# Performance work log

Hardware: AMD Instinct MI355X
Metric: run time of the kernel (lower is better)

Reference implementation:

```python
import jax, jax.numpy as jnp
import numpy as np

N_HEADS = 32
N_KV_HEADS = 8
HEAD_DIM = 64
ROPE_BASE = 10000.0


def setup_inputs() -> dict:
    key = jax.random.key(0)
    ks = jax.random.split(key, 5)
    B, T, C = 4, 1024, 2048
    kv_dim = N_KV_HEADS * HEAD_DIM
    scale = 0.02
    return {
        "x": jax.random.normal(ks[0], (B, T, C), dtype=jnp.float32),
        "Wq": jax.random.normal(ks[1], (C, C), dtype=jnp.float32) * scale,
        "Wk": jax.random.normal(ks[2], (C, kv_dim), dtype=jnp.float32) * scale,
        "Wv": jax.random.normal(ks[3], (C, kv_dim), dtype=jnp.float32) * scale,
        "Wp": jax.random.normal(ks[4], (C, C), dtype=jnp.float32) * scale,
    }


def _rotate_half(x):
    # interleaved rotation: (x0,x1,x2,x3,...) -> (-x1,x0,-x3,x2,...)
    x1 = x[..., ::2]
    x2 = x[..., 1::2]
    return jnp.stack((-x2, x1), axis=-1).reshape(x.shape)


def _rope_tables(T, dtype):
    inv_freq = 1.0 / (ROPE_BASE ** (jnp.arange(0, HEAD_DIM, 2, dtype=jnp.float32) / HEAD_DIM))
    freqs = jnp.arange(T, dtype=jnp.float32)[:, None] * inv_freq[None, :]  # (T, D/2)
    cos = jnp.repeat(jnp.cos(freqs), 2, axis=-1).astype(dtype)  # (T, D)
    sin = jnp.repeat(jnp.sin(freqs), 2, axis=-1).astype(dtype)
    return cos[None, None], sin[None, None]  # (1,1,T,D)


def reference(x, Wq, Wk, Wv, Wp):
    B, T, C = x.shape
    H, KV, D = N_HEADS, N_KV_HEADS, HEAD_DIM
    q = (x @ Wq).reshape(B, T, H, D).transpose(0, 2, 1, 3)   # (B,H,T,D)
    k = (x @ Wk).reshape(B, T, KV, D).transpose(0, 2, 1, 3)  # (B,KV,T,D)
    v = (x @ Wv).reshape(B, T, KV, D).transpose(0, 2, 1, 3)

    cos, sin = _rope_tables(T, x.dtype)
    q = q * cos + _rotate_half(q) * sin
    k = k * cos + _rotate_half(k) * sin

    rf = H // KV
    k = jnp.repeat(k, rf, axis=1)  # (B,H,T,D) GQA broadcast
    v = jnp.repeat(v, rf, axis=1)

    scores = jnp.einsum('bhqd,bhkd->bhqk', q, k) / jnp.sqrt(jnp.asarray(D, x.dtype))
    causal = jnp.tril(jnp.ones((T, T), dtype=bool))
    scores = jnp.where(causal[None, None], scores, -jnp.inf)
    attn = jax.nn.softmax(scores, axis=-1)
    out = jnp.einsum('bhqk,bhkd->bhqd', attn, v)  # (B,H,T,D)
    out = out.transpose(0, 2, 1, 3).reshape(B, T, C)
    return out @ Wp
```

## Files before the change

### kernel.cpp

```cpp
#include <hip/hip_runtime.h>
#include <hip/hip_bf16.h>


typedef __attribute__((ext_vector_type(4))) float f32x4;
typedef __attribute__((ext_vector_type(8))) short short8;

#define AS1C(p) ((const __attribute__((address_space(1))) void*)(p))
#define AS3(p)  ((__attribute__((address_space(3))) void*)(p))

__device__ __forceinline__ unsigned short f2bf(float f) {
  union { float f; unsigned int u; } x; x.f = f;
  unsigned int r = x.u + 0x7FFFu + ((x.u >> 16) & 1u);
  return (unsigned short)(r >> 16);
}

__device__ __forceinline__ unsigned short bfc(float f) {
  return __bfloat16_as_ushort(__float2bfloat16(f));
}

__device__ __forceinline__ float ex2(float x) {
  return __builtin_amdgcn_exp2f(x);
}

__global__ void rope_tab_kernel(float2* __restrict__ tab) {
  const int idx = blockIdx.x * 256 + threadIdx.x;
  const int t = idx >> 5, i = idx & 31;
  const float invf = exp2f(-(float)i * 0.41524101186092029f);
  float sv, cv;
  __sincosf((float)t * invf, &sv, &cv);
  tab[idx] = make_float2(cv, sv);
}

__global__ void cvt_bf16_kernel(const float* __restrict__ src,
                                unsigned short* __restrict__ dst, int n4) {
  int i = blockIdx.x * blockDim.x + threadIdx.x;
  if (i >= n4) return;
  const f32x4 v = *(const f32x4*)(src + (size_t)i * 4);
  ushort4 u = make_ushort4(f2bf(v[0]), f2bf(v[1]), f2bf(v[2]), f2bf(v[3]));
  *(ushort4*)(dst + (size_t)i * 4) = u;
}

__global__ void transpose_qkv_w_kernel(const float* __restrict__ Wq,
                                       const float* __restrict__ Wk,
                                       const float* __restrict__ Wv,
                                       unsigned short* __restrict__ dst) {
  __shared__ float tile[32][33];
  const int z = blockIdx.z;
  const float* src;
  int N, rowOff;
  float scale;
  if (z == 0)      { src = Wq; N = 2048; rowOff = 0;    scale = 0.18033688011112042f; }
  else if (z == 1) { src = Wk; N = 512;  rowOff = 2048; scale = 1.0f; }
  else             { src = Wv; N = 512;  rowOff = 2560; scale = 1.0f; }
  const int n0 = blockIdx.x * 32, k0 = blockIdx.y * 32;
  if (n0 >= N) return;
  const int tx = threadIdx.x & 31, ty = threadIdx.x >> 5;
#pragma unroll
  for (int i = ty; i < 32; i += 8)
    tile[i][tx] = src[(size_t)(k0 + i) * N + (n0 + tx)];
  __syncthreads();
#pragma unroll
  for (int i = ty; i < 32; i += 8)
    dst[(size_t)(rowOff + n0 + i) * 2048 + (k0 + tx)] = f2bf(tile[tx][i] * scale);
}

__global__ void transpose_bf16_kernel(const float* __restrict__ src,
                                      unsigned short* __restrict__ dst,
                                      int N, int rowOff, float scale) {
  __shared__ float tile[32][33];
  const int n0 = blockIdx.x * 32, k0 = blockIdx.y * 32;
  const int tx = threadIdx.x & 31, ty = threadIdx.x >> 5;
#pragma unroll
  for (int i = ty; i < 32; i += 8)
    tile[i][tx] = src[(size_t)(k0 + i) * N + (n0 + tx)];
  __syncthreads();
#pragma unroll
  for (int i = ty; i < 32; i += 8)
    dst[(size_t)(rowOff + n0 + i) * 2048 + (k0 + tx)] = f2bf(tile[tx][i] * scale);
}

__global__ void rope_cvt2_kernel(const float2* __restrict__ tab,
                                 const float* __restrict__ qkf,
                                 unsigned short* __restrict__ qb,
                                 unsigned short* __restrict__ kb) {
  const int idx = blockIdx.x * 256 + threadIdx.x;
  const int m = idx / 320;
  const int p = idx - m * 320;
  const int t = m & 1023;
  unsigned short* dst;
  int srcCol, dcol;
  if (p < 256) { dcol = p * 8; srcCol = dcol; dst = qb + (size_t)m * 2048 + dcol; }
  else         { dcol = (p - 256) * 8; srcCol = 2048 + dcol; dst = kb + (size_t)m * 512 + dcol; }
  const int i0 = (srcCol & 63) >> 1;
  const float* src = qkf + (size_t)m * 2560 + srcCol;
  const f32x4 v0 = *(const f32x4*)(src);
  const f32x4 v1 = *(const f32x4*)(src + 4);
  float x[8] = {v0[0], v0[1], v0[2], v0[3], v1[0], v1[1], v1[2], v1[3]};
  short8 o;
#pragma unroll
  for (int j = 0; j < 4; ++j) {
    const float2 cs = tab[t * 32 + i0 + j];
    const float x1 = x[2 * j], x2 = x[2 * j + 1];
    o[2 * j]     = (short)bfc(x1 * cs.x - x2 * cs.y);
    o[2 * j + 1] = (short)bfc(x2 * cs.x + x1 * cs.y);
  }
  *(short8*)dst = o;
}

#define GEMM_CORE(A_, Bt_, K_)                                                           \
  __shared__ unsigned short S[65536];                                                    \
  const int tid = threadIdx.x;                                                           \
  const int lane = tid & 63, w = tid >> 6;                                               \
  const int l15 = lane & 15, lg = lane >> 4;                                             \
  const int nwgx = gridDim.x;                                                            \
  const int nwg = nwgx * gridDim.y;                                                      \
  int lid = blockIdx.x + nwgx * blockIdx.y;                                              \
  lid = (lid & 7) * (nwg >> 3) + (lid >> 3);                                             \
  const int m0 = (lid / nwgx) * 256, n0 = (lid % nwgx) * 256;                            \
  const int ah = w >> 2;                                                                 \
  const int bh = (w & 3) >> 1;                                                           \
  const int bs = (w & 1) * 64;                                                           \
  const int NT = (K_) >> 6;                                                              \
  const int sr = tid >> 3;                                                               \
  const int sc = ((tid & 7) ^ (sr & 7)) << 3;                                            \
  f32x4 acc[8][4];                                                                       \
  _Pragma("unroll") for (int i = 0; i < 8; ++i)                                          \
  _Pragma("unroll") for (int j = 0; j < 4; ++j)                                          \
  _Pragma("unroll") for (int c = 0; c < 4; ++c) acc[i][j][c] = 0.f;                      \
  SB(0, 0); SB(0, 1); SA(0, 0); SA(0, 1);                                                \
  SB(1, 0); SB(1, 1); SA(1, 0); SA(1, 1);                                                \
  asm volatile("s_waitcnt vmcnt(8)" ::: "memory");                                       \
  __builtin_amdgcn_s_barrier();                                                          \
  short8 af[2][4], b0[2][2], b1[2][2];                                                   \
  for (int t = 0; t < NT; t += 2) {                                                      \
    const bool nl = (t + 2 < NT);                                                        \
    RDA(t, 0); RDB(b0, t, 0);                                                            \
    BAR();                                                                               \
    MM(0, 0, b0);                                                                        \
    BAR();                                                                               \
    RDB(b1, t, 1);                                                                       \
    BAR();                                                                               \
    MM(0, 1, b1);                                                                        \
    BAR();                                                                               \
    RDA(t, 1);                                                                           \
    if (nl) SB(t + 2, 0);                                                                \
    BAR();                                                                               \
    MM(1, 1, b1);                                                                        \
    BAR();                                                                               \
    if (nl) {                                                                            \
      SB(t + 2, 1); SA(t + 2, 0);                                                        \
      asm volatile("s_waitcnt vmcnt(6)" ::: "memory");                                   \
    } else {                                                                             \
      asm volatile("s_waitcnt vmcnt(0)" ::: "memory");                                   \
    }                                                                                    \
    BAR();                                                                               \
    MM(1, 0, b0);                                                                        \
    BAR();                                                                               \
    RDA(t + 1, 0); RDB(b0, t + 1, 0);                                                    \
    if (nl) SA(t + 2, 1);                                                                \
    BAR();                                                                               \
    MM(0, 0, b0);                                                                        \
    BAR();                                                                               \
    RDB(b1, t + 1, 1);                                                                   \
    BAR();                                                                               \
    MM(0, 1, b1);                                                                        \
    BAR();                                                                               \
    RDA(t + 1, 1);                                                                       \
    if (nl) SB(t + 3, 0);                                                                \
    BAR();                                                                               \
    MM(1, 1, b1);                                                                        \
    BAR();                                                                               \
    if (nl) {                                                                            \
      SB(t + 3, 1); SA(t + 3, 0); SA(t + 3, 1);                                          \
      asm volatile("s_waitcnt vmcnt(8)" ::: "memory");                                   \
    }                                                                                    \
    BAR();                                                                               \
    MM(1, 0, b0);                                                                        \
    BAR();                                                                               \
  }

#define SA(tile, half)                                                                   \
  do {                                                                                   \
    const unsigned short* p_ = Ap + (size_t)(m0 + (half) * 128 + sr) * Kd + (tile) * 64 + sc; \
    const int d_ = (((tile) & 1) << 14) + ((half) << 13) + tid * 8;                      \
    __builtin_amdgcn_global_load_lds(AS1C(p_), AS3(&S[d_]), 16, 0, 0);                   \
    __builtin_amdgcn_global_load_lds(AS1C(p_ + (size_t)64 * Kd), AS3(&S[d_ + 4096]), 16, 0, 0); \
  } while (0)

#define SB(tile, half)                                                                   \
  do {                                                                                   \
    const unsigned short* p_ = Bp + (size_t)(n0 + (half) * 128 + sr) * Kd + (tile) * 64 + sc; \
    const int d_ = 32768 + (((tile) & 1) << 14) + ((half) << 13) + tid * 8;              \
    __builtin_amdgcn_global_load_lds(AS1C(p_), AS3(&S[d_]), 16, 0, 0);                   \
    __builtin_amdgcn_global_load_lds(AS1C(p_ + (size_t)64 * Kd), AS3(&S[d_ + 4096]), 16, 0, 0); \
  } while (0)

#define RDA(tile, Msub)                                                                  \
  _Pragma("unroll") for (int kk = 0; kk < 2; ++kk)                                       \
  _Pragma("unroll") for (int fm = 0; fm < 4; ++fm) {                                     \
    const int r_ = (Msub) * 64 + fm * 16 + l15;                                          \
    af[kk][fm] = *(const short8*)&S[(((tile) & 1) << 14) + (ah << 13) + r_ * 64 +        \
                                    (((kk << 2) | lg) ^ (r_ & 7)) * 8];                  \
  }

#define RDB(dst, tile, Nsub)                                                             \
  _Pragma("unroll") for (int kk = 0; kk < 2; ++kk)                                       \
  _Pragma("unroll") for (int j = 0; j < 2; ++j) {                                        \
    const int r_ = bs + ((Nsub) * 2 + j) * 16 + l15;                                     \
    dst[kk][j] = *(const short8*)&S[32768 + (((tile) & 1) << 14) + (bh << 13) + r_ * 64 +\
                                    (((kk << 2) | lg) ^ (r_ & 7)) * 8];                  \
  }

#define MM(Msub, Nsub, bb)                                                               \
  do {                                                                                   \
    __builtin_amdgcn_s_setprio(1);                                                       \
    _Pragma("unroll") for (int kk = 0; kk < 2; ++kk)                                     \
    _Pragma("unroll") for (int fm = 0; fm < 4; ++fm)                                     \
    _Pragma("unroll") for (int j = 0; j < 2; ++j)                                        \
      acc[(Msub) * 4 + fm][(Nsub) * 2 + j] = __builtin_amdgcn_mfma_f32_16x16x32_bf16(    \
          af[kk][fm], bb[kk][j], acc[(Msub) * 4 + fm][(Nsub) * 2 + j], 0, 0, 0);         \
    __builtin_amdgcn_s_setprio(0);                                                       \
  } while (0)

#define BAR() __builtin_amdgcn_s_barrier()

__global__ __launch_bounds__(512, 2) void gemm256_qkv_kernel(
    const unsigned short* __restrict__ Ap, const unsigned short* __restrict__ Bp,
    float* __restrict__ qkf, unsigned short* __restrict__ vt) {
  const int Kd = 2048;
  GEMM_CORE(Ap, Bp, Kd)

  const int colbase = n0 + (w & 3) * 64;
  if (n0 >= 2560) {
#pragma unroll
    for (int fm8 = 0; fm8 < 8; ++fm8) {
      const int row = m0 + ah * 128 + (fm8 >> 2) * 64 + (fm8 & 3) * 16 + lg * 4;
      const int z = (row >> 10) * 8 + ((colbase - 2560) >> 6);
      const int t0 = row & 1023;
#pragma unroll
      for (int fn4 = 0; fn4 < 4; ++fn4) {
        const int d = (colbase + fn4 * 16 + l15 - 2560) & 63;
        ushort4 u = make_ushort4(bfc(acc[fm8][fn4][0]), bfc(acc[fm8][fn4][1]),
                                 bfc(acc[fm8][fn4][2]), bfc(acc[fm8][fn4][3]));
        *(ushort4*)&vt[(size_t)z * 65536 + d * 1024 + t0] = u;
      }
    }
  } else {
#pragma unroll
    for (int fm8 = 0; fm8 < 8; ++fm8) {
      const int row = m0 + ah * 128 + (fm8 >> 2) * 64 + (fm8 & 3) * 16 + lg * 4;
#pragma unroll
      for (int fn4 = 0; fn4 < 4; ++fn4) {
        const size_t base = (size_t)row * 2560 + colbase + fn4 * 16 + l15;
#pragma unroll
        for (int r = 0; r < 4; ++r) qkf[base + (size_t)r * 2560] = acc[fm8][fn4][r];
      }
    }
  }
}

#define SA2(tile, half)                                                                  \
  do {                                                                                   \
    const unsigned short* p_ = Ap + (size_t)(m0 + (half) * 128 + sr) * Kd + (tile) * 64 + sc; \
    const int d_ = (((tile) & 1) << 14) + ((half) << 13) + tid * 8;                      \
    __builtin_amdgcn_global_load_lds(AS1C(p_), AS3(&S[d_]), 16, 0, 0);                   \
    __builtin_amdgcn_global_load_lds(AS1C(p_ + (size_t)64 * Kd), AS3(&S[d_ + 4096]), 16, 0, 0); \
  } while (0)

#define SB2(tile)                                                                        \
  do {                                                                                   \
    const unsigned short* p_ = Bp + (size_t)(n0 + sr) * Kd + (tile) * 64 + sc;           \
    const int d_ = 32768 + (((tile) & 1) << 13) + tid * 8;                               \
    __builtin_amdgcn_global_load_lds(AS1C(p_), AS3(&S[d_]), 16, 0, 0);                   \
    __builtin_amdgcn_global_load_lds(AS1C(p_ + (size_t)64 * Kd), AS3(&S[d_ + 4096]), 16, 0, 0); \
  } while (0)

#define RDA2(tile, Msub)                                                                 \
  _Pragma("unroll") for (int kk = 0; kk < 2; ++kk)                                       \
  _Pragma("unroll") for (int fm = 0; fm < 4; ++fm) {                                     \
    const int r_ = (Msub) * 64 + fm * 16 + l15;                                          \
    af[kk][fm] = *(const short8*)&S[(((tile) & 1) << 14) + (ah << 13) + r_ * 64 +        \
                                    (((kk << 2) | lg) ^ (r_ & 7)) * 8];                  \
  }

#define RDB2(dst, tile)                                                                  \
  _Pragma("unroll") for (int kk = 0; kk < 2; ++kk)                                       \
  _Pragma("unroll") for (int j = 0; j < 2; ++j) {                                        \
    const int r_ = wn + j * 16 + l15;                                                    \
    dst[kk][j] = *(const short8*)&S[32768 + (((tile) & 1) << 13) + r_ * 64 +             \
                                    (((kk << 2) | lg) ^ (r_ & 7)) * 8];                  \
  }

#define MM2(Msub, bb)                                                                    \
  do {                                                                                   \
    __builtin_amdgcn_s_setprio(1);                                                       \
    _Pragma("unroll") for (int kk = 0; kk < 2; ++kk)                                     \
    _Pragma("unroll") for (int fm = 0; fm < 4; ++fm)                                     \
    _Pragma("unroll") for (int j = 0; j < 2; ++j)                                        \
      acc[(Msub) * 4 + fm][j] = __builtin_amdgcn_mfma_f32_16x16x32_bf16(                 \
          af[kk][fm], bb[kk][j], acc[(Msub) * 4 + fm][j], 0, 0, 0);                      \
    __builtin_amdgcn_s_setprio(0);                                                       \
  } while (0)

__global__ __launch_bounds__(512, 1) void gemm256x128_kernel(
    const unsigned short* __restrict__ Ap, const unsigned short* __restrict__ Bp,
    float* __restrict__ C, int K, int N) {
  __shared__ unsigned short S[49152];
  const int tid = threadIdx.x;
  const int lane = tid & 63, w = tid >> 6;
  const int l15 = lane & 15, lg = lane >> 4;
  const int nwgx = gridDim.x;
  const int nwg = nwgx * gridDim.y;
  int lid = blockIdx.x + nwgx * blockIdx.y;
  lid = (lid & 7) * (nwg >> 3) + (lid >> 3);
  const int m0 = (lid / nwgx) * 256, n0 = (lid % nwgx) * 128;
  const int ah = w >> 2;
  const int wn = (w & 3) * 32;
  const int NT = K >> 6;
  const int Kd = K;
  const int sr = tid >> 3;
  const int sc = ((tid & 7) ^ (sr & 7)) << 3;

  f32x4 acc[8][2];
#pragma unroll
  for (int i = 0; i < 8; ++i)
#pragma unroll
    for (int j = 0; j < 2; ++j)
#pragma unroll
      for (int c = 0; c < 4; ++c) acc[i][j][c] = 0.f;

  SB2(0); SA2(0, 0); SA2(0, 1); SB2(1); SA2(1, 0);
  asm volatile("s_waitcnt vmcnt(4)" ::: "memory");
  __builtin_amdgcn_s_barrier();

  short8 af[2][4], b0[2][2], b1[2][2];

  for (int t = 0; t < NT; t += 2) {
    const bool nl = (t + 2 < NT);
    RDA2(t, 0); RDB2(b0, t);
    SA2(t + 1, 1);
    BAR();
    MM2(0, b0);
    BAR();
    RDA2(t, 1);
    if (nl) {
      SB2(t + 2); SA2(t + 2, 0);
      asm volatile("s_waitcnt vmcnt(4)" ::: "memory");
    } else {
      asm volatile("s_waitcnt vmcnt(0)" ::: "memory");
    }
    BAR();
    MM2(1, b0);
    BAR();
    RDA2(t + 1, 0); RDB2(b1, t + 1);
    if (nl) SA2(t + 2, 1);
    BAR();
    MM2(0, b1);
    BAR();
    RDA2(t + 1, 1);
    if (nl) {
      SB2(t + 3); SA2(t + 3, 0);
      asm volatile("s_waitcnt vmcnt(4)" ::: "memory");
    }
    BAR();
    MM2(1, b1);
    BAR();
  }

#pragma unroll
  for (int fm8 = 0; fm8 < 8; ++fm8)
#pragma unroll
    for (int j = 0; j < 2; ++j) {
      const size_t base =
          (size_t)(m0 + ah * 128 + (fm8 >> 2) * 64 + (fm8 & 3) * 16 + lg * 4) * N +
          (n0 + wn + j * 16 + l15);
#pragma unroll
      for (int r = 0; r < 4; ++r) C[base + (size_t)r * N] = acc[fm8][j][r];
    }
}

__global__ __launch_bounds__(256) void attn_mfma_kernel(
    const unsigned short* __restrict__ qb, const unsigned short* __restrict__ kb,
    const unsigned short* __restrict__ vt, unsigned short* __restrict__ attnb) {
  int lid = blockIdx.x + 8 * (blockIdx.y + 32 * blockIdx.z);
  lid = (lid & 7) * 128 + (lid >> 3);
  const int bx = lid & 7, h = (lid >> 3) & 31, b = lid >> 8;
  const int kvh = h >> 2;
  __shared__ unsigned short S[20480];
  const int tid = threadIdx.x, lane = tid & 63, w = tid >> 6;
  const int l15 = lane & 15, lg = lane >> 4;
  const int rowbase = w * 16 + lg * 4;

  const int gi0 = w * 64 + lane;
  const int r0 = gi0 >> 3, g0 = (gi0 & 7) ^ (r0 & 7);
  const int gi1 = (4 + w) * 64 + lane;
  const int r1 = gi1 >> 3, g1 = (gi1 & 7) ^ (r1 & 7);

  const unsigned short* kbase = kb + (size_t)b * 1024 * 512 + kvh * 64;
  const unsigned short* vbase = vt + (size_t)(b * 8 + kvh) * 64 * 1024;

#define STAGE_KV(kOff, vOff, jj)                                                    \
  do {                                                                              \
    __builtin_amdgcn_global_load_lds(AS1C(kbase + ((jj) * 64 + r0) * 512 + g0 * 8), \
                                     AS3(&S[(kOff) + w * 512]), 16, 0, 0);          \
    __builtin_amdgcn_global_load_lds(AS1C(kbase + ((jj) * 64 + r1) * 512 + g1 * 8), \
                                     AS3(&S[(kOff) + (4 + w) * 512]), 16, 0, 0);    \
    __builtin_amdgcn_global_load_lds(AS1C(vbase + r0 * 1024 + (jj) * 64 + g0 * 8),  \
                                     AS3(&S[(vOff) + w * 512]), 16, 0, 0);          \
    __builtin_amdgcn_global_load_lds(AS1C(vbase + r1 * 1024 + (jj) * 64 + g1 * 8),  \
                                     AS3(&S[(vOff) + (4 + w) * 512]), 16, 0, 0);    \
  } while (0)

#define STAGE_Q(qt)                                                                     \
  do {                                                                                  \
    const size_t qr_ = (size_t)b * 1024 + (qt) * 64;                                    \
    __builtin_amdgcn_global_load_lds(AS1C(qb + (qr_ + r0) * 2048 + h * 64 + g0 * 8),    \
                                     AS3(&S[w * 512]), 16, 0, 0);                       \
    __builtin_amdgcn_global_load_lds(AS1C(qb + (qr_ + r1) * 2048 + h * 64 + g1 * 8),    \
                                     AS3(&S[(4 + w) * 512]), 16, 0, 0);                 \
  } while (0)

  const int qts0 = bx, qts1 = 15 - bx;

  short8 ones;
#pragma unroll
  for (int i = 0; i < 8; ++i) ones[i] = (short)0x3F80;

  STAGE_Q(qts0);
  STAGE_KV(4096, 12288, 0);
  __syncthreads();

  int g = 0;
  for (int sub = 0; sub < 2; ++sub) {
    const int qtc = sub ? qts1 : qts0;
    const size_t qrow0 = (size_t)b * 1024 + qtc * 64;

    short8 qf[2];
#pragma unroll
    for (int kk = 0; kk < 2; ++kk) {
      const int r = w * 16 + l15;
      const int gq = ((kk << 2) | lg) ^ (r & 7);
      qf[kk] = *(const short8*)&S[r * 64 + gq * 8];
    }

    f32x4 oa[4], oe;
#pragma unroll
    for (int r = 0; r < 4; ++r) oe[r] = 0.f;
#pragma unroll
    for (int fd = 0; fd < 4; ++fd)
#pragma unroll
      for (int r = 0; r < 4; ++r) oa[fd][r] = 0.f;

    for (int j = 0; j <= qtc; ++j, ++g) {
      const int cur = g & 1;
      const int kOff = 4096 + cur * 4096;
      const int vOff = 12288 + cur * 4096;
      if (g < 16) {
        const int nj = (g + 1 <= qts0) ? g + 1 : g - qts0;
        STAGE_KV(4096 + (cur ^ 1) * 4096, 12288 + (cur ^ 1) * 4096, nj);
      }

      f32x4 sa[4];
#pragma unroll
      for (int fn = 0; fn < 4; ++fn)
#pragma unroll
        for (int r = 0; r < 4; ++r) sa[fn][r] = 0.f;
#pragma unroll
      for (int kk = 0; kk < 2; ++kk) {
        short8 kf[4];
#pragma unroll
        for (int fn = 0; fn < 4; ++fn) {
          const int rkv = fn * 16 + l15;
          const int gk = ((kk << 2) | lg) ^ (rkv & 7);
          kf[fn] = *(const short8*)&S[kOff + rkv * 64 + gk * 8];
        }
        __builtin_amdgcn_s_setprio(1);
#pragma unroll
        for (int fn = 0; fn < 4; ++fn)
          sa[fn] = __builtin_amdgcn_mfma_f32_16x16x32_bf16(qf[kk], kf[fn], sa[fn], 0, 0, 0);
        __builtin_amdgcn_s_setprio(0);
      }

      if (j == qtc) {
#pragma unroll
        for (int r = 0; r < 4; ++r) {
          const int row = rowbase + r;
#pragma unroll
          for (int fn = 0; fn < 4; ++fn)
            if ((fn * 16 + l15) > row) sa[fn][r] = -INFINITY;
        }
      }
#pragma unroll
      for (int fn = 0; fn < 4; ++fn)
#pragma unroll
        for (int r = 0; r < 4; ++r) sa[fn][r] = ex2(sa[fn][r]);

#pragma unroll
      for (int r = 0; r < 4; ++r) {
        const int prow = rowbase + r;
#pragma unroll
        for (int fn = 0; fn < 4; ++fn) {
          const int col = fn * 16 + l15;
          const int gp = (col >> 3) ^ (prow & 7);
          S[prow * 64 + gp * 8 + (col & 7)] = bfc(sa[fn][r]);
        }
      }

#pragma unroll
      for (int kk = 0; kk < 2; ++kk) {
        const int rp = w * 16 + l15;
        const int gp = ((kk << 2) | lg) ^ (rp & 7);
        const short8 pf = *(const short8*)&S[rp * 64 + gp * 8];
        short8 vf[4];
#pragma unroll
        for (int fd = 0; fd < 4; ++fd) {
          const int rd = fd * 16 + l15;
          const int gv = ((kk << 2) | lg) ^ (rd & 7);
          vf[fd] = *(const short8*)&S[vOff + rd * 64 + gv * 8];
        }
        __builtin_amdgcn_s_setprio(1);
#pragma unroll
        for (int fd = 0; fd < 4; ++fd)
          oa[fd] = __builtin_amdgcn_mfma_f32_16x16x32_bf16(pf, vf[fd], oa[fd], 0, 0, 0);
        oe = __builtin_amdgcn_mfma_f32_16x16x32_bf16(pf, ones, oe, 0, 0, 0);
        __builtin_amdgcn_s_setprio(0);
      }

      __syncthreads();
    }

#pragma unroll
    for (int r = 0; r < 4; ++r) {
      const float inv = 1.0f / oe[r];
      const size_t row = qrow0 + rowbase + r;
#pragma unroll
      for (int fd = 0; fd < 4; ++fd)
        attnb[row * 2048 + h * 64 + fd * 16 + l15] = f2bf(oa[fd][r] * inv);
    }

    if (sub == 0) {
      STAGE_Q(qts1);
      __syncthreads();
    }
  }
#undef STAGE_KV
#undef STAGE_Q
}

extern "C" void kernel_launch(void* const* d_in, const int* in_sizes, int n_in,
                              void* d_out, int out_size, void* d_ws, size_t ws_size,
                              hipStream_t stream) {
  (void)in_sizes; (void)n_in; (void)out_size; (void)ws_size;
  const float* x  = (const float*)d_in[0];
  const float* Wq = (const float*)d_in[1];
  const float* Wk = (const float*)d_in[2];
  const float* Wv = (const float*)d_in[3];
  const float* Wp = (const float*)d_in[4];

  char* w = (char*)d_ws;
  unsigned short* xb    = (unsigned short*)(w);
  unsigned short* Wt    = (unsigned short*)(w + 16777216);
  unsigned short* Wpt   = (unsigned short*)(w + 29360128);
  float*          qkf   = (float*)(w + 37748736);
  unsigned short* vtb   = (unsigned short*)(w + 79691776);
  unsigned short* attnb = (unsigned short*)(w + 83886080);
  float2*         rtab  = (float2*)(w + 100663296);
  unsigned short* qb    = (unsigned short*)(w);
  unsigned short* kbuf  = (unsigned short*)(w + 16777216);
  float* out = (float*)d_out;

  rope_tab_kernel<<<128, 256, 0, stream>>>(rtab);
  cvt_bf16_kernel<<<8192, 256, 0, stream>>>(x, xb, 2097152);
  transpose_qkv_w_kernel<<<dim3(64, 64, 3), 256, 0, stream>>>(Wq, Wk, Wv, Wt);
  transpose_bf16_kernel<<<dim3(64, 64), 256, 0, stream>>>(Wp, Wpt, 2048, 0, 1.0f);

  gemm256_qkv_kernel<<<dim3(12, 16), 512, 0, stream>>>(xb, Wt, qkf, vtb);
  rope_cvt2_kernel<<<5120, 256, 0, stream>>>(rtab, qkf, qb, kbuf);
  attn_mfma_kernel<<<dim3(8, 32, 4), 256, 0, stream>>>(qb, kbuf, vtb, attnb);
  gemm256x128_kernel<<<dim3(16, 16), 512, 0, stream>>>(attnb, Wpt, out, 2048, 2048);
}
```

Measured before the change: 177.3 us.

## Retile QKV GEMM to 256x192 tiles for a 256-block grid

Replaces the 256x256 QKV projection GEMM (192 workgroups) with a 256x192 tile variant launched on a 16x16 grid, giving 256 workgroups that map more evenly onto the device's compute units. The wave layout changes to 4x2 warps each owning 64x96 outputs, the LDS staging and prefetch schedule are rewritten for three B sub-tiles per K step, and launch bounds drop to one block per CU. The aim is to cut tail imbalance from a partial last wave. The cost is a smaller tile with less operand reuse per load, lower occupancy, and a more intricate vmcnt wait schedule that must stay correct.

```diff
diff --git a/kernel.cpp b/kernel.cpp
--- a/kernel.cpp
+++ b/kernel.cpp
@@ -107,153 +107,145 @@
   *(short8*)dst = o;
 }
 
-#define GEMM_CORE(A_, Bt_, K_)                                                           \
-  __shared__ unsigned short S[65536];                                                    \
-  const int tid = threadIdx.x;                                                           \
-  const int lane = tid & 63, w = tid >> 6;                                               \
-  const int l15 = lane & 15, lg = lane >> 4;                                             \
-  const int nwgx = gridDim.x;                                                            \
-  const int nwg = nwgx * gridDim.y;                                                      \
-  int lid = blockIdx.x + nwgx * blockIdx.y;                                              \
-  lid = (lid & 7) * (nwg >> 3) + (lid >> 3);                                             \
-  const int m0 = (lid / nwgx) * 256, n0 = (lid % nwgx) * 256;                            \
-  const int ah = w >> 2;                                                                 \
-  const int bh = (w & 3) >> 1;                                                           \
-  const int bs = (w & 1) * 64;                                                           \
-  const int NT = (K_) >> 6;                                                              \
-  const int sr = tid >> 3;                                                               \
-  const int sc = ((tid & 7) ^ (sr & 7)) << 3;                                            \
-  f32x4 acc[8][4];                                                                       \
-  _Pragma("unroll") for (int i = 0; i < 8; ++i)                                          \
-  _Pragma("unroll") for (int j = 0; j < 4; ++j)                                          \
-  _Pragma("unroll") for (int c = 0; c < 4; ++c) acc[i][j][c] = 0.f;                      \
-  SB(0, 0); SB(0, 1); SA(0, 0); SA(0, 1);                                                \
-  SB(1, 0); SB(1, 1); SA(1, 0); SA(1, 1);                                                \
-  asm volatile("s_waitcnt vmcnt(8)" ::: "memory");                                       \
-  __builtin_amdgcn_s_barrier();                                                          \
-  short8 af[2][4], b0[2][2], b1[2][2];                                                   \
-  for (int t = 0; t < NT; t += 2) {                                                      \
-    const bool nl = (t + 2 < NT);                                                        \
-    RDA(t, 0); RDB(b0, t, 0);                                                            \
-    BAR();                                                                               \
-    MM(0, 0, b0);                                                                        \
-    BAR();                                                                               \
-    RDB(b1, t, 1);                                                                       \
-    BAR();                                                                               \
-    MM(0, 1, b1);                                                                        \
-    BAR();                                                                               \
-    RDA(t, 1);                                                                           \
-    if (nl) SB(t + 2, 0);                                                                \
-    BAR();                                                                               \
-    MM(1, 1, b1);                                                                        \
-    BAR();                                                                               \
-    if (nl) {                                                                            \
-      SB(t + 2, 1); SA(t + 2, 0);                                                        \
-      asm volatile("s_waitcnt vmcnt(6)" ::: "memory");                                   \
-    } else {                                                                             \
-      asm volatile("s_waitcnt vmcnt(0)" ::: "memory");                                   \
-    }                                                                                    \
-    BAR();                                                                               \
-    MM(1, 0, b0);                                                                        \
-    BAR();                                                                               \
-    RDA(t + 1, 0); RDB(b0, t + 1, 0);                                                    \
-    if (nl) SA(t + 2, 1);                                                                \
-    BAR();                                                                               \
-    MM(0, 0, b0);                                                                        \
-    BAR();                                                                               \
-    RDB(b1, t + 1, 1);                                                                   \
-    BAR();                                                                               \
-    MM(0, 1, b1);                                                                        \
-    BAR();                                                                               \
-    RDA(t + 1, 1);                                                                       \
-    if (nl) SB(t + 3, 0);                                                                \
-    BAR();                                                                               \
-    MM(1, 1, b1);                                                                        \
-    BAR();                                                                               \
-    if (nl) {                                                                            \
-      SB(t + 3, 1); SA(t + 3, 0); SA(t + 3, 1);                                          \
-      asm volatile("s_waitcnt vmcnt(8)" ::: "memory");                                   \
-    }                                                                                    \
-    BAR();                                                                               \
-    MM(1, 0, b0);                                                                        \
-    BAR();                                                                               \
-  }
-
-#define SA(tile, half)                                                                   \
+#define BAR() __builtin_amdgcn_s_barrier()
+
+#define SA3(tile, half)                                                                  \
   do {                                                                                   \
-    const unsigned short* p_ = Ap + (size_t)(m0 + (half) * 128 + sr) * Kd + (tile) * 64 + sc; \
+    const unsigned short* p_ = Ap + (size_t)(m0 + (half) * 128 + sr) * 2048 + (tile) * 64 + sc; \
     const int d_ = (((tile) & 1) << 14) + ((half) << 13) + tid * 8;                      \
     __builtin_amdgcn_global_load_lds(AS1C(p_), AS3(&S[d_]), 16, 0, 0);                   \
-    __builtin_amdgcn_global_load_lds(AS1C(p_ + (size_t)64 * Kd), AS3(&S[d_ + 4096]), 16, 0, 0); \
-  } while (0)
-
-#define SB(tile, half)                                                                   \
+    __builtin_amdgcn_global_load_lds(AS1C(p_ + (size_t)64 * 2048), AS3(&S[d_ + 4096]), 16, 0, 0); \
+  } while (0)
+
+#define SB3(tile, u)                                                                     \
   do {                                                                                   \
-    const unsigned short* p_ = Bp + (size_t)(n0 + (half) * 128 + sr) * Kd + (tile) * 64 + sc; \
-    const int d_ = 32768 + (((tile) & 1) << 14) + ((half) << 13) + tid * 8;              \
+    const unsigned short* p_ = Bp + (size_t)(n0 + (u) * 64 + sr) * 2048 + (tile) * 64 + sc; \
+    const int d_ = 32768 + ((tile) & 1) * 12288 + (u) * 4096 + tid * 8;                  \
     __builtin_amdgcn_global_load_lds(AS1C(p_), AS3(&S[d_]), 16, 0, 0);                   \
-    __builtin_amdgcn_global_load_lds(AS1C(p_ + (size_t)64 * Kd), AS3(&S[d_ + 4096]), 16, 0, 0); \
-  } while (0)
-
-#define RDA(tile, Msub)                                                                  \
+  } while (0)
+
+#define RDA3(tile)                                                                       \
   _Pragma("unroll") for (int kk = 0; kk < 2; ++kk)                                       \
   _Pragma("unroll") for (int fm = 0; fm < 4; ++fm) {                                     \
-    const int r_ = (Msub) * 64 + fm * 16 + l15;                                          \
-    af[kk][fm] = *(const short8*)&S[(((tile) & 1) << 14) + (ah << 13) + r_ * 64 +        \
+    const int r_ = mg * 64 + fm * 16 + l15;                                              \
+    af[kk][fm] = *(const short8*)&S[(((tile) & 1) << 14) + r_ * 64 +                     \
                                     (((kk << 2) | lg) ^ (r_ & 7)) * 8];                  \
   }
 
-#define RDB(dst, tile, Nsub)                                                             \
+#define RDB3(tile, p)                                                                    \
   _Pragma("unroll") for (int kk = 0; kk < 2; ++kk)                                       \
-  _Pragma("unroll") for (int j = 0; j < 2; ++j) {                                        \
-    const int r_ = bs + ((Nsub) * 2 + j) * 16 + l15;                                     \
-    dst[kk][j] = *(const short8*)&S[32768 + (((tile) & 1) << 14) + (bh << 13) + r_ * 64 +\
+  _Pragma("unroll") for (int jj = 0; jj < 2; ++jj) {                                     \
+    const int r_ = ng * 96 + ((p) * 2 + jj) * 16 + l15;                                  \
+    bf[kk][jj] = *(const short8*)&S[32768 + ((tile) & 1) * 12288 + r_ * 64 +             \
                                     (((kk << 2) | lg) ^ (r_ & 7)) * 8];                  \
   }
 
-#define MM(Msub, Nsub, bb)                                                               \
+#define MM3(p)                                                                           \
   do {                                                                                   \
     __builtin_amdgcn_s_setprio(1);                                                       \
     _Pragma("unroll") for (int kk = 0; kk < 2; ++kk)                                     \
     _Pragma("unroll") for (int fm = 0; fm < 4; ++fm)                                     \
-    _Pragma("unroll") for (int j = 0; j < 2; ++j)                                        \
-      acc[(Msub) * 4 + fm][(Nsub) * 2 + j] = __builtin_amdgcn_mfma_f32_16x16x32_bf16(    \
-          af[kk][fm], bb[kk][j], acc[(Msub) * 4 + fm][(Nsub) * 2 + j], 0, 0, 0);         \
+    _Pragma("unroll") for (int jj = 0; jj < 2; ++jj)                                     \
+      acc[fm][(p) * 2 + jj] = __builtin_amdgcn_mfma_f32_16x16x32_bf16(                   \
+          af[kk][fm], bf[kk][jj], acc[fm][(p) * 2 + jj], 0, 0, 0);                       \
     __builtin_amdgcn_s_setprio(0);                                                       \
   } while (0)
 
-#define BAR() __builtin_amdgcn_s_barrier()
-
-__global__ __launch_bounds__(512, 2) void gemm256_qkv_kernel(
+__global__ __launch_bounds__(512, 1) void gemm256x192_qkv_kernel(
     const unsigned short* __restrict__ Ap, const unsigned short* __restrict__ Bp,
     float* __restrict__ qkf, unsigned short* __restrict__ vt) {
-  const int Kd = 2048;
-  GEMM_CORE(Ap, Bp, Kd)
-
-  const int colbase = n0 + (w & 3) * 64;
-  if (n0 >= 2560) {
-#pragma unroll
-    for (int fm8 = 0; fm8 < 8; ++fm8) {
-      const int row = m0 + ah * 128 + (fm8 >> 2) * 64 + (fm8 & 3) * 16 + lg * 4;
-      const int z = (row >> 10) * 8 + ((colbase - 2560) >> 6);
-      const int t0 = row & 1023;
-#pragma unroll
-      for (int fn4 = 0; fn4 < 4; ++fn4) {
-        const int d = (colbase + fn4 * 16 + l15 - 2560) & 63;
-        ushort4 u = make_ushort4(bfc(acc[fm8][fn4][0]), bfc(acc[fm8][fn4][1]),
-                                 bfc(acc[fm8][fn4][2]), bfc(acc[fm8][fn4][3]));
+  __shared__ unsigned short S[57344];
+  const int tid = threadIdx.x;
+  const int lane = tid & 63, w = tid >> 6;
+  const int l15 = lane & 15, lg = lane >> 4;
+  int lid = blockIdx.x + 16 * blockIdx.y;
+  lid = (lid & 7) * 32 + (lid >> 3);
+  const int m0 = (lid >> 4) * 256, n0 = (lid & 15) * 192;
+  const int mg = w >> 1;
+  const int ng = w & 1;
+  const int sr = tid >> 3;
+  const int sc = ((tid & 7) ^ (sr & 7)) << 3;
+  const int NT = 32;
+
+  f32x4 acc[4][6];
+#pragma unroll
+  for (int i = 0; i < 4; ++i)
+#pragma unroll
+    for (int j = 0; j < 6; ++j)
+#pragma unroll
+      for (int c = 0; c < 4; ++c) acc[i][j][c] = 0.f;
+
+  SA3(0, 0); SA3(0, 1); SB3(0, 0); SB3(0, 1); SB3(0, 2);
+  SA3(1, 0); SA3(1, 1); SB3(1, 0);
+  asm volatile("s_waitcnt vmcnt(5)" ::: "memory");
+  BAR();
+
+  short8 af[2][4], bf[2][2];
+
+  for (int t = 0; t < NT; t += 2) {
+    const bool nl = (t + 2 < NT);
+    RDA3(t); RDB3(t, 0);
+    SB3(t + 1, 1); SB3(t + 1, 2);
+    BAR();
+    MM3(0);
+    BAR();
+    RDB3(t, 1);
+    if (nl) SA3(t + 2, 0);
+    BAR();
+    MM3(1);
+    BAR();
+    RDB3(t, 2);
+    if (nl) {
+      SA3(t + 2, 1); SB3(t + 2, 0);
+      asm volatile("s_waitcnt vmcnt(5)" ::: "memory");
+    } else {
+      asm volatile("s_waitcnt vmcnt(0)" ::: "memory");
+    }
+    BAR();
+    MM3(2);
+    BAR();
+    RDA3(t + 1); RDB3(t + 1, 0);
+    if (nl) { SB3(t + 2, 1); SB3(t + 2, 2); }
+    BAR();
+    MM3(0);
+    BAR();
+    RDB3(t + 1, 1);
+    if (nl) SA3(t + 3, 0);
+    BAR();
+    MM3(1);
+    BAR();
+    RDB3(t + 1, 2);
+    if (nl) {
+      SA3(t + 3, 1); SB3(t + 3, 0);
+      asm volatile("s_waitcnt vmcnt(5)" ::: "memory");
+    }
+    BAR();
+    MM3(2);
+    BAR();
+  }
+
+#pragma unroll
+  for (int fn = 0; fn < 6; ++fn) {
+    const int col16 = n0 + ng * 96 + fn * 16;
+    if (col16 < 2560) {
+#pragma unroll
+      for (int fm = 0; fm < 4; ++fm) {
+        const int row = m0 + mg * 64 + fm * 16 + lg * 4;
+        const size_t base = (size_t)row * 2560 + col16 + l15;
+#pragma unroll
+        for (int r = 0; r < 4; ++r) qkf[base + (size_t)r * 2560] = acc[fm][fn][r];
+      }
+    } else {
+      const int dz = (col16 - 2560) >> 6;
+      const int d = ((col16 - 2560) & 63) + l15;
+#pragma unroll
+      for (int fm = 0; fm < 4; ++fm) {
+        const int row = m0 + mg * 64 + fm * 16 + lg * 4;
+        const int z = (row >> 10) * 8 + dz;
+        const int t0 = row & 1023;
+        ushort4 u = make_ushort4(bfc(acc[fm][fn][0]), bfc(acc[fm][fn][1]),
+                                 bfc(acc[fm][fn][2]), bfc(acc[fm][fn][3]));
         *(ushort4*)&vt[(size_t)z * 65536 + d * 1024 + t0] = u;
-      }
-    }
-  } else {
-#pragma unroll
-    for (int fm8 = 0; fm8 < 8; ++fm8) {
-      const int row = m0 + ah * 128 + (fm8 >> 2) * 64 + (fm8 & 3) * 16 + lg * 4;
-#pragma unroll
-      for (int fn4 = 0; fn4 < 4; ++fn4) {
-        const size_t base = (size_t)row * 2560 + colbase + fn4 * 16 + l15;
-#pragma unroll
-        for (int r = 0; r < 4; ++r) qkf[base + (size_t)r * 2560] = acc[fm8][fn4][r];
       }
     }
   }
@@ -574,7 +566,7 @@
   transpose_qkv_w_kernel<<<dim3(64, 64, 3), 256, 0, stream>>>(Wq, Wk, Wv, Wt);
   transpose_bf16_kernel<<<dim3(64, 64), 256, 0, stream>>>(Wp, Wpt, 2048, 0, 1.0f);
 
-  gemm256_qkv_kernel<<<dim3(12, 16), 512, 0, stream>>>(xb, Wt, qkf, vtb);
+  gemm256x192_qkv_kernel<<<dim3(16, 16), 512, 0, stream>>>(xb, Wt, qkf, vtb);
   rope_cvt2_kernel<<<5120, 256, 0, stream>>>(rtab, qkf, qb, kbuf);
   attn_mfma_kernel<<<dim3(8, 32, 4), 256, 0, stream>>>(qb, kbuf, vtb, attnb);
   gemm256x128_kernel<<<dim3(16, 16), 512, 0, stream>>>(attnb, Wpt, out, 2048, 2048);
```

Measured after the change: 166.2 us. 6.2% less time.
